# Kernel optimization log

Measured on AMD Instinct MI355X. Metric: run time of the kernel, lower is better.

Reference implementation:

```python
import jax, jax.numpy as jnp
import numpy as np

D_MODEL = 1024
N_HEADS = 16
D_HEAD = D_MODEL // N_HEADS
EPS = 1e-5


def setup_inputs() -> dict:
    key = jax.random.key(0)
    ks = jax.random.split(key, 7)
    B, T = 4, 2048
    s = 1.0 / np.sqrt(D_MODEL)
    return {
        "x": jax.random.normal(ks[0], (B, T, D_MODEL), dtype=jnp.float32),
        "ln_g": jnp.ones((D_MODEL,), jnp.float32),
        "ln_b": jnp.zeros((D_MODEL,), jnp.float32),
        "W_qkv": jax.random.normal(ks[1], (D_MODEL, 3 * D_MODEL), jnp.float32) * s,
        "b_qkv": jnp.zeros((3 * D_MODEL,), jnp.float32),
        "W_gate": jax.random.normal(ks[2], (D_MODEL, D_MODEL), jnp.float32) * s,
        "b_gate": jnp.zeros((D_MODEL,), jnp.float32),
        "W_proj": jax.random.normal(ks[3], (D_MODEL, D_MODEL), jnp.float32) * s,
        "b_proj": jnp.zeros((D_MODEL,), jnp.float32),
    }


def _forward(x, ln_g, ln_b, W_qkv, b_qkv, W_gate, b_gate, W_proj, b_proj):
    B, T, D = x.shape
    H, d = N_HEADS, D_HEAD
    # LayerNorm (eps=1e-5, biased variance as in torch)
    mu = jnp.mean(x, axis=-1, keepdims=True)
    var = jnp.mean((x - mu) ** 2, axis=-1, keepdims=True)
    x_norm = (x - mu) * jax.lax.rsqrt(var + EPS) * ln_g + ln_b
    qkv = x_norm @ W_qkv + b_qkv
    q, k, v = jnp.split(qkv, 3, axis=-1)  # each [B,T,D]
    # concept gate uses raw x
    gate = jax.nn.sigmoid(x @ W_gate + b_gate)
    gate = gate / (jnp.mean(gate, axis=-1, keepdims=True) + EPS)
    q = (q * gate).reshape(B, T, H, d)
    k = (k * gate).reshape(B, T, H, d)
    v = v.reshape(B, T, H, d)
    # ReLU^2 feature map in fp32
    q = jax.nn.relu(q.astype(jnp.float32)) ** 2 + EPS
    k = jax.nn.relu(k.astype(jnp.float32)) ** 2 + EPS
    v = v.astype(jnp.float32)
    # causal linear attention via kv recurrence (scan over T, T-major)
    qT = jnp.transpose(q, (1, 0, 2, 3))  # [T,B,H,d]
    kT = jnp.transpose(k, (1, 0, 2, 3))
    vT = jnp.transpose(v, (1, 0, 2, 3))

    def step(carry, inp):
        kv_s, k_s = carry  # [B,H,d,d], [B,H,d]
        q_t, k_t, v_t = inp  # [B,H,d]
        kv_s = kv_s + k_t[..., :, None] * v_t[..., None, :]
        k_s = k_s + k_t
        num = jnp.einsum('bhd,bhdm->bhm', q_t, kv_s)
        den = jnp.einsum('bhd,bhd->bh', q_t, k_s)[..., None] + EPS
        return (kv_s, k_s), num / den

    init = (jnp.zeros((B, H, d, d), jnp.float32), jnp.zeros((B, H, d), jnp.float32))
    _, outT = jax.lax.scan(step, init, (qT, kT, vT))  # [T,B,H,d]
    out = jnp.transpose(outT, (1, 0, 2, 3)).astype(x.dtype).reshape(B, T, D)
    return out @ W_proj + b_proj


def reference(x, ln_g, ln_b, W_qkv, b_qkv, W_gate, b_gate, W_proj, b_proj):
    return _forward(x, ln_g, ln_b, W_qkv, b_qkv, W_gate, b_gate, W_proj, b_proj)
```

## Files before the change

kernel.cpp:

```cpp
#include <hip/hip_runtime.h>
#include <math.h>

#define TOK 8192
#define DM 1024
#define EPSF 1e-5f

typedef __attribute__((ext_vector_type(8))) short short8;
typedef __attribute__((ext_vector_type(4))) float f32x4;

static __device__ __forceinline__ ushort f2bf(float f) {
  unsigned u = __float_as_uint(f);
  unsigned r = (u + 0x7fffu + ((u >> 16) & 1u)) >> 16;
  return (ushort)r;
}
static __device__ __forceinline__ float bf2f(ushort u) {
  return __uint_as_float((unsigned)u << 16);
}

static __device__ __forceinline__ void gload_lds16(const ushort* g, ushort* l) {
  __builtin_amdgcn_global_load_lds((const __attribute__((address_space(1))) void*)g,
                                   (__attribute__((address_space(3))) void*)l, 16, 0, 0);
}

static __device__ __forceinline__ int cswz(int row) {
  return (((row & 7) ^ ((row >> 3) & 7)) << 3);
}

static __device__ __forceinline__ int2 xcd_remap(int nx) {
  int bid = blockIdx.y * nx + blockIdx.x;
  int nwg = nx * gridDim.y;
  int cpx = nwg >> 3;
  int id = (bid & 7) * cpx + (bid >> 3);
  return make_int2(id % nx, id / nx);
}

__global__ __launch_bounds__(256) void lncvt_k(const float* __restrict__ x,
                                               const float* __restrict__ g,
                                               const float* __restrict__ b,
                                               ushort* __restrict__ x_b,
                                               ushort* __restrict__ xn_b) {
  __shared__ float red[8];
  int row = blockIdx.x;
  const float4* xr = (const float4*)(x + (size_t)row * DM);
  float4 v = xr[threadIdx.x];
  ushort4 xb4;
  xb4.x = f2bf(v.x); xb4.y = f2bf(v.y); xb4.z = f2bf(v.z); xb4.w = f2bf(v.w);
  ((ushort4*)(x_b + (size_t)row * DM))[threadIdx.x] = xb4;
  float s = v.x + v.y + v.z + v.w;
#pragma unroll
  for (int o = 32; o > 0; o >>= 1) s += __shfl_down(s, o, 64);
  int lane = threadIdx.x & 63, w = threadIdx.x >> 6;
  if (lane == 0) red[w] = s;
  __syncthreads();
  float mu = (red[0] + red[1] + red[2] + red[3]) * (1.0f / DM);
  float dx = v.x - mu, dy = v.y - mu, dz = v.z - mu, dw = v.w - mu;
  float ss = dx * dx + dy * dy + dz * dz + dw * dw;
#pragma unroll
  for (int o = 32; o > 0; o >>= 1) ss += __shfl_down(ss, o, 64);
  if (lane == 0) red[4 + w] = ss;
  __syncthreads();
  float var = (red[4] + red[5] + red[6] + red[7]) * (1.0f / DM);
  float rstd = rsqrtf(var + EPSF);
  float4 gg = ((const float4*)g)[threadIdx.x];
  float4 bb = ((const float4*)b)[threadIdx.x];
  ushort4 o4;
  o4.x = f2bf(dx * rstd * gg.x + bb.x);
  o4.y = f2bf(dy * rstd * gg.y + bb.y);
  o4.z = f2bf(dz * rstd * gg.z + bb.z);
  o4.w = f2bf(dw * rstd * gg.w + bb.w);
  ((ushort4*)(xn_b + (size_t)row * DM))[threadIdx.x] = o4;
}

__global__ __launch_bounds__(256) void tconv_k(const float* __restrict__ W,
                                               ushort* __restrict__ Wt, int K, int N) {
  __shared__ ushort tile[32][33];
  int k0 = blockIdx.y * 32, n0 = blockIdx.x * 32;
  int tx = threadIdx.x & 31, ty = threadIdx.x >> 5;
#pragma unroll
  for (int i = 0; i < 4; i++) {
    int k = ty + i * 8;
    tile[k][tx] = f2bf(W[(size_t)(k0 + k) * N + n0 + tx]);
  }
  __syncthreads();
#pragma unroll
  for (int i = 0; i < 4; i++) {
    int n = ty + i * 8;
    Wt[(size_t)(n0 + n) * K + k0 + tx] = tile[tx][n];
  }
}

__global__ __launch_bounds__(256) void rowinv_k(const ushort* __restrict__ gate_b,
                                                float* __restrict__ ginv) {
  int row = blockIdx.x * 4 + (threadIdx.x >> 6);
  int l = threadIdx.x & 63;
  const short8* gr = (const short8*)(gate_b + (size_t)row * DM);
  short8 g0 = gr[l * 2], g1 = gr[l * 2 + 1];
  float s = 0.f;
#pragma unroll
  for (int j = 0; j < 8; j++) s += bf2f((ushort)g0[j]) + bf2f((ushort)g1[j]);
#pragma unroll
  for (int o = 1; o < 64; o <<= 1) s += __shfl_xor(s, o, 64);
  if (l == 0) ginv[row] = 1.0f / (s * (1.0f / DM) + EPSF);
}

#define BM 128
#define BN 128
#define BK 64
__global__ __launch_bounds__(256) void gemm_bf16_k(
    const ushort* __restrict__ A, const ushort* __restrict__ Bt,
    const float* __restrict__ bias, float* __restrict__ Cf,
    ushort* __restrict__ Cb, int ldc, int K, int mode) {
  __shared__ __align__(16) ushort As[BM * BK];
  __shared__ __align__(16) ushort Bs[BN * BK];
  int tid = threadIdx.x, lane = tid & 63, w = tid >> 6;
  int2 bxy = xcd_remap(gridDim.x);
  int m0 = bxy.y * BM, n0 = bxy.x * BN;
  int wr = w >> 1, wc = w & 1;
  f32x4 acc[4][4] = {};
  for (int k0 = 0; k0 < K; k0 += BK) {
#pragma unroll
    for (int j = 0; j < 4; j++) {
      int lu = (w * 4 + j) * 64 + lane;
      int r = lu >> 3;
      int kb = (lu & 7) ^ (r & 7);
      gload_lds16(A + (size_t)(m0 + r) * K + k0 + kb * 8, &As[(w * 4 + j) * 512]);
      gload_lds16(Bt + (size_t)(n0 + r) * K + k0 + kb * 8, &Bs[(w * 4 + j) * 512]);
    }
    __syncthreads();
#pragma unroll
    for (int ks = 0; ks < 2; ks++) {
      short8 af[4], bfr[4];
      int kq = ks * 4 + (lane >> 4);
#pragma unroll
      for (int f = 0; f < 4; f++) {
        int ra = wr * 64 + f * 16 + (lane & 15);
        af[f] = *(const short8*)&As[(ra * 8 + (kq ^ (ra & 7))) * 8];
        int rb = wc * 64 + f * 16 + (lane & 15);
        bfr[f] = *(const short8*)&Bs[(rb * 8 + (kq ^ (rb & 7))) * 8];
      }
#pragma unroll
      for (int i = 0; i < 4; i++)
#pragma unroll
        for (int j2 = 0; j2 < 4; j2++)
          acc[i][j2] = __builtin_amdgcn_mfma_f32_16x16x32_bf16(af[i], bfr[j2], acc[i][j2], 0, 0, 0);
    }
    __syncthreads();
  }
#pragma unroll
  for (int i = 0; i < 4; i++) {
#pragma unroll
    for (int j2 = 0; j2 < 4; j2++) {
      int col = n0 + wc * 64 + j2 * 16 + (lane & 15);
      float bv = bias[col];
#pragma unroll
      for (int r = 0; r < 4; r++) {
        int row = m0 + wr * 64 + i * 16 + (lane >> 4) * 4 + r;
        float v = acc[i][j2][r] + bv;
        if (mode == 2) {
          v = 1.0f / (1.0f + expf(-v));
          Cb[(size_t)row * ldc + col] = f2bf(v);
        } else {
          Cf[(size_t)row * ldc + col] = v;
        }
      }
    }
  }
}

__global__ __launch_bounds__(256) void gemm_qkv_k(
    const ushort* __restrict__ A, const ushort* __restrict__ Bt,
    const float* __restrict__ bias, const ushort* __restrict__ gate_b,
    const float* __restrict__ ginv,
    ushort* __restrict__ qb, ushort* __restrict__ kb,
    ushort* __restrict__ kt, ushort* __restrict__ vt, int K) {
  __shared__ __align__(16) ushort sh[16896];
  __shared__ float ginvs[128];
  ushort* As = sh;
  ushort* Bs = sh + BM * BK;
  int tid = threadIdx.x, lane = tid & 63, w = tid >> 6;
  int2 bxy = xcd_remap(gridDim.x);
  int m0 = bxy.y * BM, n0 = bxy.x * BN;
  int wr = w >> 1, wc = w & 1;
  f32x4 acc[4][4] = {};
  for (int k0 = 0; k0 < K; k0 += BK) {
#pragma unroll
    for (int j = 0; j < 4; j++) {
      int lu = (w * 4 + j) * 64 + lane;
      int r = lu >> 3;
      int kb2 = (lu & 7) ^ (r & 7);
      gload_lds16(A + (size_t)(m0 + r) * K + k0 + kb2 * 8, &As[(w * 4 + j) * 512]);
      gload_lds16(Bt + (size_t)(n0 + r) * K + k0 + kb2 * 8, &Bs[(w * 4 + j) * 512]);
    }
    __syncthreads();
#pragma unroll
    for (int ks = 0; ks < 2; ks++) {
      short8 af[4], bfr[4];
      int kq = ks * 4 + (lane >> 4);
#pragma unroll
      for (int f = 0; f < 4; f++) {
        int ra = wr * 64 + f * 16 + (lane & 15);
        af[f] = *(const short8*)&As[(ra * 8 + (kq ^ (ra & 7))) * 8];
        int rb = wc * 64 + f * 16 + (lane & 15);
        bfr[f] = *(const short8*)&Bs[(rb * 8 + (kq ^ (rb & 7))) * 8];
      }
#pragma unroll
      for (int i = 0; i < 4; i++)
#pragma unroll
        for (int j2 = 0; j2 < 4; j2++)
          acc[i][j2] = __builtin_amdgcn_mfma_f32_16x16x32_bf16(af[i], bfr[j2], acc[i][j2], 0, 0, 0);
    }
    __syncthreads();
  }
  int region = n0 >> 10;
  int n0b = n0 & 1023;
  int h0 = n0b >> 6;
  if (region < 2) {
    if (tid < 128) ginvs[tid] = ginv[m0 + tid];
#pragma unroll
    for (int it = 0; it < 8; it++) {
      int e = it * 256 + tid;
      int row = e >> 4, ch = e & 15;
      *(short8*)&sh[row * 132 + ch * 8] =
          *(const short8*)&gate_b[(size_t)(m0 + row) * DM + n0b + ch * 8];
    }
    __syncthreads();
#pragma unroll
    for (int i = 0; i < 4; i++) {
#pragma unroll
      for (int j2 = 0; j2 < 4; j2++) {
        int cl = wc * 64 + j2 * 16 + (lane & 15);
        float bv = bias[n0 + cl];
        int rl0 = wr * 64 + i * 16 + (lane >> 4) * 4;
#pragma unroll
        for (int r = 0; r < 4; r++) {
          float gv = bf2f(sh[(rl0 + r) * 132 + cl]) * ginvs[rl0 + r];
          float v = (acc[i][j2][r] + bv) * gv;
          v = fmaxf(v, 0.0f);
          acc[i][j2][r] = v * v + EPSF;
        }
      }
    }
    __syncthreads();
  } else {
#pragma unroll
    for (int i = 0; i < 4; i++)
#pragma unroll
      for (int j2 = 0; j2 < 4; j2++) {
        int cl = wc * 64 + j2 * 16 + (lane & 15);
        float bv = bias[n0 + cl];
#pragma unroll
        for (int r = 0; r < 4; r++) acc[i][j2][r] += bv;
      }
  }
#pragma unroll
  for (int i = 0; i < 4; i++) {
#pragma unroll
    for (int j2 = 0; j2 < 4; j2++) {
      int cl = wc * 64 + j2 * 16 + (lane & 15);
      int rl0 = wr * 64 + i * 16 + (lane >> 4) * 4;
#pragma unroll
      for (int r = 0; r < 4; r++) {
        int row = rl0 + r;
        sh[row * 128 + (cl ^ cswz(row))] = f2bf(acc[i][j2][r]);
      }
    }
  }
  __syncthreads();
  if (region < 2) {
    ushort* dstRM = (region == 0) ? qb : kb;
#pragma unroll
    for (int it = 0; it < 8; it++) {
      int e = it * 256 + tid;
      int row = e >> 4, ch = e & 15;
      short8 val = *(const short8*)&sh[row * 128 + ((ch * 8) ^ cswz(row))];
      int tglob = m0 + row;
      size_t bh2 = (size_t)(tglob >> 11) * 16 + h0 + (ch >> 3);
      *(short8*)&dstRM[(bh2 * 2048 + (tglob & 2047)) * 64 + (ch & 7) * 8] = val;
    }
  }
  if (region >= 1) {
    ushort* dstT = (region == 1) ? kt : vt;
#pragma unroll
    for (int it = 0; it < 8; it++) {
      int e = it * 256 + tid;
      int tch = e & 15, dkrow = e >> 4;
      short8 val;
#pragma unroll
      for (int j = 0; j < 8; j++) {
        int row = tch * 8 + j;
        val[j] = (short)sh[row * 128 + (dkrow ^ cswz(row))];
      }
      int tglob0 = m0 + tch * 8;
      size_t bh2 = (size_t)(tglob0 >> 11) * 16 + h0 + (dkrow >> 6);
      *(short8*)&dstT[(bh2 * 64 + (dkrow & 63)) * 2048 + (tglob0 & 2047)] = val;
    }
  }
}

__global__ __launch_bounds__(256) void chunkpfx_k(const ushort* __restrict__ kt,
                                                  const ushort* __restrict__ vt,
                                                  ushort* __restrict__ KVb,
                                                  float* __restrict__ ksum) {
  int dvs = blockIdx.x, bh = blockIdx.y;
  int tid = threadIdx.x, l = tid & 63, w = tid >> 6;
  int lr = l & 15, lg = l >> 4;
  const ushort* vT = vt + ((size_t)bh * 64 + dvs * 16 + lr) * 2048;
  const ushort* kT = kt + ((size_t)bh * 64 + w * 16 + lr) * 2048;
  f32x4 run = {0.f, 0.f, 0.f, 0.f};
  float runks = 0.0f;
  short8 a0 = *(const short8*)&vT[lg * 8];
  short8 a1 = *(const short8*)&vT[32 + lg * 8];
  short8 b0 = *(const short8*)&kT[lg * 8];
  short8 b1 = *(const short8*)&kT[32 + lg * 8];
  for (int c = 0; c < 32; c++) {
    ushort* dst = KVb + ((size_t)bh * 32 + c) * 4096 +
                  (size_t)(dvs * 16 + lg * 4) * 64 + w * 16 + lr;
    dst[0] = f2bf(run[0]); dst[64] = f2bf(run[1]);
    dst[128] = f2bf(run[2]); dst[192] = f2bf(run[3]);
    if (dvs == 0) {
      float s = 0.f;
#pragma unroll
      for (int j = 0; j < 8; j++) s += bf2f((ushort)b0[j]) + bf2f((ushort)b1[j]);
      s += __shfl_xor(s, 16, 64);
      s += __shfl_xor(s, 32, 64);
      if (l < 16) ksum[((size_t)bh * 32 + c) * 64 + w * 16 + l] = runks;
      runks += s;
    }
    int cn = (c + 1) & 31;
    short8 na0 = *(const short8*)&vT[cn * 64 + lg * 8];
    short8 na1 = *(const short8*)&vT[cn * 64 + 32 + lg * 8];
    short8 nb0 = *(const short8*)&kT[cn * 64 + lg * 8];
    short8 nb1 = *(const short8*)&kT[cn * 64 + 32 + lg * 8];
    run = __builtin_amdgcn_mfma_f32_16x16x32_bf16(a0, b0, run, 0, 0, 0);
    run = __builtin_amdgcn_mfma_f32_16x16x32_bf16(a1, b1, run, 0, 0, 0);
    a0 = na0; a1 = na1; b0 = nb0; b1 = nb1;
  }
}

__global__ __launch_bounds__(256) void attn_k(
    const ushort* __restrict__ qb, const ushort* __restrict__ kb,
    const ushort* __restrict__ vt, const ushort* __restrict__ KVb,
    const float* __restrict__ ks, ushort* __restrict__ attnout) {
  int c = blockIdx.x, bh = blockIdx.y;
  int b = bh >> 4, h = bh & 15;
  const ushort* qB = qb + ((size_t)bh * 2048 + (size_t)c * 64) * 64;
  const ushort* kB = kb + ((size_t)bh * 2048 + (size_t)c * 64) * 64;
  const ushort* vT = vt + (size_t)bh * 64 * 2048 + (size_t)c * 64;
  const ushort* kvB = KVb + ((size_t)bh * 32 + c) * 4096;
  const float* ksP = ks + ((size_t)bh * 32 + c) * 64;
  __shared__ __align__(16) char SL[64 * 128];
  __shared__ float denp[4][64];
  __shared__ float den2p[4][64];
  __shared__ float invden[64];
  int tid = threadIdx.x, l = tid & 63, w = tid >> 6;
  int lr = l & 15, lg = l >> 4;
  {
    short8 q0 = *(const short8*)&qB[(size_t)l * 64 + w * 16];
    short8 q1 = *(const short8*)&qB[(size_t)l * 64 + w * 16 + 8];
    float d2 = 0.0f;
#pragma unroll
    for (int j = 0; j < 8; j++) {
      d2 += bf2f((ushort)q0[j]) * ksP[w * 16 + j];
      d2 += bf2f((ushort)q1[j]) * ksP[w * 16 + 8 + j];
    }
    den2p[w][l] = d2;
  }
#pragma unroll
  for (int n = 0; n < 4; n++) {
    f32x4 sa = {0.f, 0.f, 0.f, 0.f};
#pragma unroll
    for (int g = 0; g < 2; g++) {
      short8 a = *(const short8*)&kB[(size_t)(w * 16 + lr) * 64 + g * 32 + lg * 8];
      short8 bq = *(const short8*)&qB[(size_t)(n * 16 + lr) * 64 + g * 32 + lg * 8];
      sa = __builtin_amdgcn_mfma_f32_16x16x32_bf16(a, bq, sa, 0, 0, 0);
    }
    int t = n * 16 + lr;
    int s0 = w * 16 + lg * 4;
    float dsum = 0.0f;
    ushort sb[4];
#pragma unroll
    for (int r = 0; r < 4; r++) {
      float v = (s0 + r <= t) ? sa[r] : 0.0f;
      dsum += v;
      sb[r] = f2bf(v);
    }
    dsum += __shfl_xor(dsum, 16, 64);
    dsum += __shfl_xor(dsum, 32, 64);
    if (l < 16) denp[w][n * 16 + l] = dsum;
    int u = (s0 >> 3) ^ (t & 7);
    uint2 p;
    p.x = sb[0] | ((unsigned)sb[1] << 16);
    p.y = sb[2] | ((unsigned)sb[3] << 16);
    *(uint2*)&SL[t * 128 + u * 16 + (s0 & 7) * 2] = p;
  }
  __syncthreads();
  if (tid < 64) {
    float den = denp[0][tid] + denp[1][tid] + denp[2][tid] + denp[3][tid] +
                den2p[0][tid] + den2p[1][tid] + den2p[2][tid] + den2p[3][tid] + EPSF;
    invden[tid] = 1.0f / den;
  }
  __syncthreads();
#pragma unroll
  for (int n = 0; n < 4; n++) {
    f32x4 oa = {0.f, 0.f, 0.f, 0.f};
#pragma unroll
    for (int g = 0; g < 2; g++) {
      short8 a = *(const short8*)&kvB[(size_t)(w * 16 + lr) * 64 + g * 32 + lg * 8];
      short8 bq = *(const short8*)&qB[(size_t)(n * 16 + lr) * 64 + g * 32 + lg * 8];
      oa = __builtin_amdgcn_mfma_f32_16x16x32_bf16(a, bq, oa, 0, 0, 0);
    }
    int t = n * 16 + lr;
#pragma unroll
    for (int g = 0; g < 2; g++) {
      short8 a = *(const short8*)&vT[(size_t)(w * 16 + lr) * 2048 + g * 32 + lg * 8];
      int u = (g * 4 + lg) ^ (t & 7);
      short8 bs = *(const short8*)&SL[t * 128 + u * 16];
      oa = __builtin_amdgcn_mfma_f32_16x16x32_bf16(a, bs, oa, 0, 0, 0);
    }
    float iv = invden[t];
    ushort ob[4];
#pragma unroll
    for (int r = 0; r < 4; r++) ob[r] = f2bf(oa[r] * iv);
    size_t tok = (size_t)b * 2048 + (size_t)c * 64 + t;
    uint2 p;
    p.x = ob[0] | ((unsigned)ob[1] << 16);
    p.y = ob[2] | ((unsigned)ob[3] << 16);
    *(uint2*)&attnout[tok * 1024 + h * 64 + w * 16 + lg * 4] = p;
  }
}

extern "C" void kernel_launch(void* const* d_in, const int* in_sizes, int n_in,
                              void* d_out, int out_size, void* d_ws, size_t ws_size,
                              hipStream_t stream) {
  const float* x      = (const float*)d_in[0];
  const float* ln_g   = (const float*)d_in[1];
  const float* ln_b   = (const float*)d_in[2];
  const float* W_qkv  = (const float*)d_in[3];
  const float* b_qkv  = (const float*)d_in[4];
  const float* W_gate = (const float*)d_in[5];
  const float* b_gate = (const float*)d_in[6];
  const float* W_proj = (const float*)d_in[7];
  const float* b_proj = (const float*)d_in[8];
  float* out = (float*)d_out;

  char* wsb = (char*)d_ws;
  const size_t TD = (size_t)TOK * DM;
  const size_t SLOT = TD * 2;
  ushort* x_b     = (ushort*)(wsb + 0 * SLOT);
  ushort* attnout = (ushort*)(wsb + 0 * SLOT);
  ushort* xn_b    = (ushort*)(wsb + 1 * SLOT);
  ushort* qb      = (ushort*)(wsb + 2 * SLOT);
  ushort* kb      = (ushort*)(wsb + 3 * SLOT);
  ushort* kt      = (ushort*)(wsb + 4 * SLOT);
  ushort* vt      = (ushort*)(wsb + 5 * SLOT);
  ushort* gate_b  = (ushort*)(wsb + 6 * SLOT);
  ushort* Wt_gate = (ushort*)(wsb + 8 * SLOT);
  ushort* Wt_qkv  = (ushort*)(wsb + 8 * SLOT);
  ushort* KVb     = (ushort*)(wsb + 8 * SLOT);
  ushort* Wt_proj = (ushort*)(wsb + 9 * SLOT);
  float*  ksum    = (float*)(wsb + 9 * SLOT + 8 * 1024 * 1024);
  float*  ginv    = (float*)(wsb + 9 * SLOT + 12 * 1024 * 1024);

  lncvt_k<<<TOK, 256, 0, stream>>>(x, ln_g, ln_b, x_b, xn_b);
  tconv_k<<<dim3(DM / 32, DM / 32), 256, 0, stream>>>(W_gate, Wt_gate, DM, DM);
  gemm_bf16_k<<<dim3(DM / BN, TOK / BM), 256, 0, stream>>>(x_b, Wt_gate, b_gate, nullptr,
                                                           gate_b, DM, DM, 2);
  rowinv_k<<<TOK / 4, 256, 0, stream>>>(gate_b, ginv);
  tconv_k<<<dim3(3 * DM / 32, DM / 32), 256, 0, stream>>>(W_qkv, Wt_qkv, DM, 3 * DM);
  gemm_qkv_k<<<dim3(3 * DM / BN, TOK / BM), 256, 0, stream>>>(xn_b, Wt_qkv, b_qkv, gate_b,
                                                              ginv, qb, kb, kt, vt, DM);
  chunkpfx_k<<<dim3(4, 64), 256, 0, stream>>>(kt, vt, KVb, ksum);
  tconv_k<<<dim3(DM / 32, DM / 32), 256, 0, stream>>>(W_proj, Wt_proj, DM, DM);
  attn_k<<<dim3(32, 64), 256, 0, stream>>>(qb, kb, vt, KVb, ksum, attnout);
  gemm_bf16_k<<<dim3(DM / BN, TOK / BM), 256, 0, stream>>>(attnout, Wt_proj, b_proj, out,
                                                           nullptr, DM, DM, 0);
}
```

Measured before the change: 211.7 us.

## Double-buffer GEMM LDS tiles, merge weight transposes, drop XCD remap

Both 128x128 GEMM kernels now use a double-buffered shared-memory ring, so the next K-tile is loaded while MFMAs run on the current one. This cuts one barrier per iteration but doubles LDS use, which can lower occupancy. The three weight transpose/convert launches are merged into one 5120-block launch, and the chunk prefix kernel uses a 1-D grid remapped so that blocks sharing a head land on the same XCD. The XCD remap is removed from the GEMMs, and the sigmoid switches to the fast __expf; Wt_gate is moved to avoid overlapping Wt_qkv.

```diff
diff --git a/kernel.cpp b/kernel.cpp
--- a/kernel.cpp
+++ b/kernel.cpp
@@ -24,14 +24,6 @@
 
 static __device__ __forceinline__ int cswz(int row) {
   return (((row & 7) ^ ((row >> 3) & 7)) << 3);
-}
-
-static __device__ __forceinline__ int2 xcd_remap(int nx) {
-  int bid = blockIdx.y * nx + blockIdx.x;
-  int nwg = nx * gridDim.y;
-  int cpx = nwg >> 3;
-  int id = (bid & 7) * cpx + (bid >> 3);
-  return make_int2(id % nx, id / nx);
 }
 
 __global__ __launch_bounds__(256) void lncvt_k(const float* __restrict__ x,
@@ -71,10 +63,18 @@
   ((ushort4*)(xn_b + (size_t)row * DM))[threadIdx.x] = o4;
 }
 
-__global__ __launch_bounds__(256) void tconv_k(const float* __restrict__ W,
-                                               ushort* __restrict__ Wt, int K, int N) {
+__global__ __launch_bounds__(256) void tconv_all_k(
+    const float* __restrict__ Wg, const float* __restrict__ Wq,
+    const float* __restrict__ Wp, ushort* __restrict__ Wtg,
+    ushort* __restrict__ Wtq, ushort* __restrict__ Wtp) {
   __shared__ ushort tile[32][33];
-  int k0 = blockIdx.y * 32, n0 = blockIdx.x * 32;
+  int bid = blockIdx.x;
+  const float* W; ushort* Wt; int N; int local;
+  if (bid < 1024)      { W = Wg; Wt = Wtg; N = 1024; local = bid; }
+  else if (bid < 4096) { W = Wq; Wt = Wtq; N = 3072; local = bid - 1024; }
+  else                 { W = Wp; Wt = Wtp; N = 1024; local = bid - 4096; }
+  int ntiles = N >> 5;
+  int n0 = (local % ntiles) * 32, k0 = (local / ntiles) * 32;
   int tx = threadIdx.x & 31, ty = threadIdx.x >> 5;
 #pragma unroll
   for (int i = 0; i < 4; i++) {
@@ -85,7 +85,7 @@
 #pragma unroll
   for (int i = 0; i < 4; i++) {
     int n = ty + i * 8;
-    Wt[(size_t)(n0 + n) * K + k0 + tx] = tile[tx][n];
+    Wt[(size_t)(n0 + n) * 1024 + k0 + tx] = tile[tx][n];
   }
 }
 
@@ -106,46 +106,65 @@
 #define BM 128
 #define BN 128
 #define BK 64
+
+static __device__ __forceinline__ void stage_tile128(
+    const ushort* __restrict__ A, const ushort* __restrict__ Bt,
+    int m0, int n0, int k0, int K, ushort* As, ushort* Bs, int w, int lane) {
+#pragma unroll
+  for (int j = 0; j < 4; j++) {
+    int lu = (w * 4 + j) * 64 + lane;
+    int r = lu >> 3;
+    int kb = (lu & 7) ^ (r & 7);
+    gload_lds16(A + (size_t)(m0 + r) * K + k0 + kb * 8, As + (w * 4 + j) * 512);
+    gload_lds16(Bt + (size_t)(n0 + r) * K + k0 + kb * 8, Bs + (w * 4 + j) * 512);
+  }
+}
+
+static __device__ __forceinline__ void compute_tile128(
+    const ushort* as, const ushort* bs, int wr, int wc, int lane, f32x4 acc[4][4]) {
+#pragma unroll
+  for (int ks = 0; ks < 2; ks++) {
+    short8 af[4], bfr[4];
+    int kq = ks * 4 + (lane >> 4);
+#pragma unroll
+    for (int f = 0; f < 4; f++) {
+      int ra = wr * 64 + f * 16 + (lane & 15);
+      af[f] = *(const short8*)&as[(ra * 8 + (kq ^ (ra & 7))) * 8];
+      int rb = wc * 64 + f * 16 + (lane & 15);
+      bfr[f] = *(const short8*)&bs[(rb * 8 + (kq ^ (rb & 7))) * 8];
+    }
+#pragma unroll
+    for (int i = 0; i < 4; i++)
+#pragma unroll
+      for (int j2 = 0; j2 < 4; j2++)
+        acc[i][j2] = __builtin_amdgcn_mfma_f32_16x16x32_bf16(af[i], bfr[j2], acc[i][j2], 0, 0, 0);
+  }
+}
+
+#define GEMM_LOOP128(A_, B_, m0_, n0_, K_)                                       \
+  f32x4 acc[4][4] = {};                                                          \
+  stage_tile128(A_, B_, m0_, n0_, 0, K_, sh, sh + 16384, w, lane);               \
+  int nt = (K_) / BK;                                                            \
+  for (int t = 0; t < nt; t++) {                                                 \
+    __syncthreads();                                                             \
+    if (t + 1 < nt)                                                              \
+      stage_tile128(A_, B_, m0_, n0_, (t + 1) * BK, K_,                          \
+                    sh + ((t + 1) & 1) * 8192, sh + 16384 + ((t + 1) & 1) * 8192,\
+                    w, lane);                                                    \
+    compute_tile128(sh + (t & 1) * 8192, sh + 16384 + (t & 1) * 8192,            \
+                    wr, wc, lane, acc);                                          \
+  }                                                                              \
+  __syncthreads();
+
 __global__ __launch_bounds__(256) void gemm_bf16_k(
     const ushort* __restrict__ A, const ushort* __restrict__ Bt,
     const float* __restrict__ bias, float* __restrict__ Cf,
     ushort* __restrict__ Cb, int ldc, int K, int mode) {
-  __shared__ __align__(16) ushort As[BM * BK];
-  __shared__ __align__(16) ushort Bs[BN * BK];
+  __shared__ __align__(16) ushort sh[32768];
   int tid = threadIdx.x, lane = tid & 63, w = tid >> 6;
-  int2 bxy = xcd_remap(gridDim.x);
-  int m0 = bxy.y * BM, n0 = bxy.x * BN;
+  int m0 = blockIdx.y * BM, n0 = blockIdx.x * BN;
   int wr = w >> 1, wc = w & 1;
-  f32x4 acc[4][4] = {};
-  for (int k0 = 0; k0 < K; k0 += BK) {
-#pragma unroll
-    for (int j = 0; j < 4; j++) {
-      int lu = (w * 4 + j) * 64 + lane;
-      int r = lu >> 3;
-      int kb = (lu & 7) ^ (r & 7);
-      gload_lds16(A + (size_t)(m0 + r) * K + k0 + kb * 8, &As[(w * 4 + j) * 512]);
-      gload_lds16(Bt + (size_t)(n0 + r) * K + k0 + kb * 8, &Bs[(w * 4 + j) * 512]);
-    }
-    __syncthreads();
-#pragma unroll
-    for (int ks = 0; ks < 2; ks++) {
-      short8 af[4], bfr[4];
-      int kq = ks * 4 + (lane >> 4);
-#pragma unroll
-      for (int f = 0; f < 4; f++) {
-        int ra = wr * 64 + f * 16 + (lane & 15);
-        af[f] = *(const short8*)&As[(ra * 8 + (kq ^ (ra & 7))) * 8];
-        int rb = wc * 64 + f * 16 + (lane & 15);
-        bfr[f] = *(const short8*)&Bs[(rb * 8 + (kq ^ (rb & 7))) * 8];
-      }
-#pragma unroll
-      for (int i = 0; i < 4; i++)
-#pragma unroll
-        for (int j2 = 0; j2 < 4; j2++)
-          acc[i][j2] = __builtin_amdgcn_mfma_f32_16x16x32_bf16(af[i], bfr[j2], acc[i][j2], 0, 0, 0);
-    }
-    __syncthreads();
-  }
+  GEMM_LOOP128(A, Bt, m0, n0, K)
 #pragma unroll
   for (int i = 0; i < 4; i++) {
 #pragma unroll
@@ -157,7 +176,7 @@
         int row = m0 + wr * 64 + i * 16 + (lane >> 4) * 4 + r;
         float v = acc[i][j2][r] + bv;
         if (mode == 2) {
-          v = 1.0f / (1.0f + expf(-v));
+          v = 1.0f / (1.0f + __expf(-v));
           Cb[(size_t)row * ldc + col] = f2bf(v);
         } else {
           Cf[(size_t)row * ldc + col] = v;
@@ -173,44 +192,12 @@
     const float* __restrict__ ginv,
     ushort* __restrict__ qb, ushort* __restrict__ kb,
     ushort* __restrict__ kt, ushort* __restrict__ vt, int K) {
-  __shared__ __align__(16) ushort sh[16896];
+  __shared__ __align__(16) ushort sh[32768];
   __shared__ float ginvs[128];
-  ushort* As = sh;
-  ushort* Bs = sh + BM * BK;
   int tid = threadIdx.x, lane = tid & 63, w = tid >> 6;
-  int2 bxy = xcd_remap(gridDim.x);
-  int m0 = bxy.y * BM, n0 = bxy.x * BN;
+  int m0 = blockIdx.y * BM, n0 = blockIdx.x * BN;
   int wr = w >> 1, wc = w & 1;
-  f32x4 acc[4][4] = {};
-  for (int k0 = 0; k0 < K; k0 += BK) {
-#pragma unroll
-    for (int j = 0; j < 4; j++) {
-      int lu = (w * 4 + j) * 64 + lane;
-      int r = lu >> 3;
-      int kb2 = (lu & 7) ^ (r & 7);
-      gload_lds16(A + (size_t)(m0 + r) * K + k0 + kb2 * 8, &As[(w * 4 + j) * 512]);
-      gload_lds16(Bt + (size_t)(n0 + r) * K + k0 + kb2 * 8, &Bs[(w * 4 + j) * 512]);
-    }
-    __syncthreads();
-#pragma unroll
-    for (int ks = 0; ks < 2; ks++) {
-      short8 af[4], bfr[4];
-      int kq = ks * 4 + (lane >> 4);
-#pragma unroll
-      for (int f = 0; f < 4; f++) {
-        int ra = wr * 64 + f * 16 + (lane & 15);
-        af[f] = *(const short8*)&As[(ra * 8 + (kq ^ (ra & 7))) * 8];
-        int rb = wc * 64 + f * 16 + (lane & 15);
-        bfr[f] = *(const short8*)&Bs[(rb * 8 + (kq ^ (rb & 7))) * 8];
-      }
-#pragma unroll
-      for (int i = 0; i < 4; i++)
-#pragma unroll
-        for (int j2 = 0; j2 < 4; j2++)
-          acc[i][j2] = __builtin_amdgcn_mfma_f32_16x16x32_bf16(af[i], bfr[j2], acc[i][j2], 0, 0, 0);
-    }
-    __syncthreads();
-  }
+  GEMM_LOOP128(A, Bt, m0, n0, K)
   int region = n0 >> 10;
   int n0b = n0 & 1023;
   int h0 = n0b >> 6;
@@ -301,11 +288,13 @@
                                                   const ushort* __restrict__ vt,
                                                   ushort* __restrict__ KVb,
                                                   float* __restrict__ ksum) {
-  int dvs = blockIdx.x, bh = blockIdx.y;
+  int bid = blockIdx.x;
+  int bh = (bid & 7) | ((bid >> 5) << 3);
+  int dvs = (bid >> 3) & 3;
   int tid = threadIdx.x, l = tid & 63, w = tid >> 6;
-  int lr = l & 15, lg = l >> 4;
-  const ushort* vT = vt + ((size_t)bh * 64 + dvs * 16 + lr) * 2048;
-  const ushort* kT = kt + ((size_t)bh * 64 + w * 16 + lr) * 2048;
+  int lg = l >> 4;
+  const ushort* vT = vt + ((size_t)bh * 64 + dvs * 16 + (l & 15)) * 2048;
+  const ushort* kT = kt + ((size_t)bh * 64 + w * 16 + (l & 15)) * 2048;
   f32x4 run = {0.f, 0.f, 0.f, 0.f};
   float runks = 0.0f;
   short8 a0 = *(const short8*)&vT[lg * 8];
@@ -314,7 +303,7 @@
   short8 b1 = *(const short8*)&kT[32 + lg * 8];
   for (int c = 0; c < 32; c++) {
     ushort* dst = KVb + ((size_t)bh * 32 + c) * 4096 +
-                  (size_t)(dvs * 16 + lg * 4) * 64 + w * 16 + lr;
+                  (size_t)(dvs * 16 + lg * 4) * 64 + w * 16 + (l & 15);
     dst[0] = f2bf(run[0]); dst[64] = f2bf(run[1]);
     dst[128] = f2bf(run[2]); dst[192] = f2bf(run[3]);
     if (dvs == 0) {
@@ -454,23 +443,21 @@
   ushort* kt      = (ushort*)(wsb + 4 * SLOT);
   ushort* vt      = (ushort*)(wsb + 5 * SLOT);
   ushort* gate_b  = (ushort*)(wsb + 6 * SLOT);
-  ushort* Wt_gate = (ushort*)(wsb + 8 * SLOT);
   ushort* Wt_qkv  = (ushort*)(wsb + 8 * SLOT);
+  ushort* Wt_gate = (ushort*)(wsb + 8 * SLOT + (size_t)8 * 1024 * 1024);
   ushort* KVb     = (ushort*)(wsb + 8 * SLOT);
   ushort* Wt_proj = (ushort*)(wsb + 9 * SLOT);
-  float*  ksum    = (float*)(wsb + 9 * SLOT + 8 * 1024 * 1024);
-  float*  ginv    = (float*)(wsb + 9 * SLOT + 12 * 1024 * 1024);
+  float*  ksum    = (float*)(wsb + 9 * SLOT + (size_t)8 * 1024 * 1024);
+  float*  ginv    = (float*)(wsb + 9 * SLOT + (size_t)12 * 1024 * 1024);
 
   lncvt_k<<<TOK, 256, 0, stream>>>(x, ln_g, ln_b, x_b, xn_b);
-  tconv_k<<<dim3(DM / 32, DM / 32), 256, 0, stream>>>(W_gate, Wt_gate, DM, DM);
+  tconv_all_k<<<5120, 256, 0, stream>>>(W_gate, W_qkv, W_proj, Wt_gate, Wt_qkv, Wt_proj);
   gemm_bf16_k<<<dim3(DM / BN, TOK / BM), 256, 0, stream>>>(x_b, Wt_gate, b_gate, nullptr,
                                                            gate_b, DM, DM, 2);
   rowinv_k<<<TOK / 4, 256, 0, stream>>>(gate_b, ginv);
-  tconv_k<<<dim3(3 * DM / 32, DM / 32), 256, 0, stream>>>(W_qkv, Wt_qkv, DM, 3 * DM);
   gemm_qkv_k<<<dim3(3 * DM / BN, TOK / BM), 256, 0, stream>>>(xn_b, Wt_qkv, b_qkv, gate_b,
                                                               ginv, qb, kb, kt, vt, DM);
-  chunkpfx_k<<<dim3(4, 64), 256, 0, stream>>>(kt, vt, KVb, ksum);
-  tconv_k<<<dim3(DM / 32, DM / 32), 256, 0, stream>>>(W_proj, Wt_proj, DM, DM);
+  chunkpfx_k<<<256, 256, 0, stream>>>(kt, vt, KVb, ksum);
   attn_k<<<dim3(32, 64), 256, 0, stream>>>(qb, kb, vt, KVb, ksum, attnout);
   gemm_bf16_k<<<dim3(DM / BN, TOK / BM), 256, 0, stream>>>(attnout, Wt_proj, b_proj, out,
                                                            nullptr, DM, DM, 0);
```

After: 194.8 us. 1.09x faster.
